# Kernel optimization log

Measured on AMD Instinct MI355X. Metric: run time of the kernel, lower is better.

The kernel has to match this reference:

```python
import jax, jax.numpy as jnp
import numpy as np

B = 4096
IN = 1024      # input_shape * 2
H = 2048       # rnn_hidden_dim * 2
A = 64         # n_actions
A2 = A * A     # fc2 output width


def setup_inputs() -> dict:
    key = jax.random.key(0)
    ks = jax.random.split(key, 12)
    s_in = 1.0 / np.sqrt(IN)
    s_h = 1.0 / np.sqrt(H)
    return {
        "inputs": jax.random.normal(ks[0], (B, IN), jnp.float32),
        "hidden_state": jax.random.normal(ks[1], (B, H), jnp.float32),
        # fc1: Linear(IN -> H)
        "W1": jax.random.uniform(ks[2], (H, IN), jnp.float32, -s_in, s_in),
        "b1": jax.random.uniform(ks[3], (H,), jnp.float32, -s_in, s_in),
        # GRUCell(H -> H), gate order r, z, n
        "Wih": jax.random.uniform(ks[4], (3 * H, H), jnp.float32, -s_h, s_h),
        "Whh": jax.random.uniform(ks[5], (3 * H, H), jnp.float32, -s_h, s_h),
        "bih": jax.random.uniform(ks[6], (3 * H,), jnp.float32, -s_h, s_h),
        "bhh": jax.random.uniform(ks[7], (3 * H,), jnp.float32, -s_h, s_h),
        # fc2: Linear(H -> A^2)
        "W2": jax.random.uniform(ks[8], (A2, H), jnp.float32, -s_h, s_h),
        "b2": jax.random.uniform(ks[9], (A2,), jnp.float32, -s_h, s_h),
    }


# Static gather indices for the vectorized __decode_combined_output.
# Row 2i, col j: max over q[i, j : j+A]  (contiguous window)
_IDX1 = np.arange(A)[:, None] + np.arange(A)[None, :]              # [A, A]
# Row 2i+1, col j: max over q[i, k-1] for k in range(j, A^2, A);
# at j=0 the index k-1 = -1 wraps to the last element (torch semantics).
_IDX2 = (np.arange(A)[:, None] + np.arange(A)[None, :] * A - 1) % A2  # [A, A]


def reference(inputs, hidden_state, W1, b1, Wih, Whh, bih, bhh, W2, b2):
    x = jax.nn.relu(inputs @ W1.T + b1)                 # [B, H]
    h_in = hidden_state.reshape(-1, H)
    gi = x @ Wih.T + bih                                # [B, 3H]
    gh = h_in @ Whh.T + bhh                             # [B, 3H]
    ir, iz, inn = jnp.split(gi, 3, axis=1)
    hr, hz, hn = jnp.split(gh, 3, axis=1)
    r = jax.nn.sigmoid(ir + hr)
    z = jax.nn.sigmoid(iz + hz)
    n = jnp.tanh(inn + r * hn)
    h = (1.0 - z) * n + z * h_in                        # [B, H]
    q = h @ W2.T + b2                                   # [B, A^2]
    q1 = jnp.max(q[:, _IDX1], axis=-1)                  # [B, A]
    q2 = jnp.max(q[:, _IDX2], axis=-1)                  # [B, A]
    out = jnp.stack([q1, q2], axis=1).reshape(-1, A)    # interleaved [2B, A]
    return out, h
```

## Files before the change

### kernel.cpp

```cpp
#include <hip/hip_runtime.h>
#include <stdint.h>

typedef unsigned short u16;
typedef __bf16 bf16x8 __attribute__((ext_vector_type(8)));
typedef float f32x4 __attribute__((ext_vector_type(4)));
typedef u16 u16x8 __attribute__((ext_vector_type(8)));

__device__ __forceinline__ float b2f(u16 v) {
    union { float f; unsigned int u; } x; x.u = ((unsigned int)v) << 16; return x.f;
}
__device__ __forceinline__ u16 f2b(float f) {
    union { float f; unsigned int u; } x; x.f = f;
    unsigned int r = x.u + 0x7fff + ((x.u >> 16) & 1);
    return (u16)(r >> 16);
}

__device__ __forceinline__ void gll16(const void* g, void* l) {
    __builtin_amdgcn_global_load_lds(
        (const __attribute__((address_space(1))) void*)g,
        (__attribute__((address_space(3))) void*)l,
        16, 0, 0);
}

__device__ __forceinline__ bf16x8 pack8(float4 f0, float4 f1) {
    union { float4 f; uint4 u; } a, b;
    a.f = f0; b.f = f1;
    const unsigned sel = 0x07060302u;
    union { unsigned u[4]; bf16x8 v; } r;
    r.u[0] = __builtin_amdgcn_perm(a.u.y + 0x8000u, a.u.x + 0x8000u, sel);
    r.u[1] = __builtin_amdgcn_perm(a.u.w + 0x8000u, a.u.z + 0x8000u, sel);
    r.u[2] = __builtin_amdgcn_perm(b.u.y + 0x8000u, b.u.x + 0x8000u, sel);
    r.u[3] = __builtin_amdgcn_perm(b.u.w + 0x8000u, b.u.z + 0x8000u, sel);
    return r.v;
}

__global__ __launch_bounds__(256) void cvt_kernel(
    const float* __restrict__ s, u16* __restrict__ d)
{
    const size_t i = ((size_t)blockIdx.x * 256 + threadIdx.x) * 8;
    float4 f0 = *(const float4*)(s + i);
    float4 f1 = *(const float4*)(s + i + 4);
    union { bf16x8 v; u16x8 u; } r;
    r.v = pack8(f0, f1);
    *(u16x8*)(d + i) = r.u;
}


#define FBAR() do { asm volatile("" ::: "memory"); \
                    __builtin_amdgcn_s_barrier();  \
                    asm volatile("" ::: "memory"); } while (0)
#define WAIT_LGKM0() asm volatile("s_waitcnt lgkmcnt(0)" ::: "memory")
#define WAIT_VM6()   asm volatile("s_waitcnt vmcnt(6)" ::: "memory")
#define WAIT_VM0()   asm volatile("s_waitcnt vmcnt(0)" ::: "memory")

__device__ __forceinline__ void stage_half(
    const u16* __restrict__ Mp, int rowBase, int K, int k0,
    u16* region, int t, int w)
{
#pragma unroll
    for (int it = 0; it < 2; ++it) {
        const int phys = it * 512 + t;
        const int r = phys >> 3;
        const int c = (phys & 7) ^ (r & 7);
        gll16(Mp + (size_t)(rowBase + r) * K + (k0 + c * 8),
              (char*)region + (it * 512 + w * 64) * 16);
    }
}

__device__ __forceinline__ void ld_a(const u16* region, int ra, int g0,
                                     bf16x8 (&out)[4][2])
{
#pragma unroll
    for (int mi = 0; mi < 4; ++mi)
#pragma unroll
        for (int s = 0; s < 2; ++s) {
            const int lr = mi * 32 + ra;
            out[mi][s] = *(const bf16x8*)((const char*)region +
                         (lr * 8 + ((s * 4 + g0) ^ (lr & 7))) * 16);
        }
}

__device__ __forceinline__ void ld_b(const u16* region, int rb, int g0,
                                     bf16x8 (&out)[2][2])
{
#pragma unroll
    for (int ni = 0; ni < 2; ++ni)
#pragma unroll
        for (int s = 0; s < 2; ++s) {
            const int lr = ni * 64 + rb;
            out[ni][s] = *(const bf16x8*)((const char*)region +
                         (lr * 8 + ((s * 4 + g0) ^ (lr & 7))) * 16);
        }
}

template <int MO, int NO>
__device__ __forceinline__ void mfma_quad(const bf16x8 (&af)[4][2],
                                          const bf16x8 (&bf)[2][2],
                                          f32x4 (&acc)[8][4])
{
    __builtin_amdgcn_s_setprio(1);
#pragma unroll
    for (int mi = 0; mi < 4; ++mi)
#pragma unroll
        for (int ni = 0; ni < 2; ++ni)
#pragma unroll
            for (int s = 0; s < 2; ++s)
                acc[MO + mi][NO + ni] = __builtin_amdgcn_mfma_f32_16x16x32_bf16(
                    af[mi][s], bf[ni][s], acc[MO + mi][NO + ni], 0, 0, 0);
    __builtin_amdgcn_s_setprio(0);
}

template <bool RELU>
__global__ __launch_bounds__(512, 2) void gemm256(
    const u16* __restrict__ A, const u16* __restrict__ Bw,
    const float* __restrict__ bias, u16* __restrict__ C,
    int M, int N, int K)
{
    (void)M;
    __shared__ alignas(16) u16 L[2][4][8192];

    const int t = threadIdx.x;
    const int l = t & 63;
    const int w = t >> 6;
    const int wr = w >> 2;
    const int wc = w & 3;

    const int gx = gridDim.x;
    const int nwg = gx * gridDim.y;
    const int orig = blockIdx.y * gx + blockIdx.x;
    const int q8 = nwg >> 3, r8 = nwg & 7;
    const int xcd = orig & 7, rem = orig >> 3;
    const int wg = (xcd < r8 ? xcd * (q8 + 1)
                             : r8 * (q8 + 1) + (xcd - r8) * q8) + rem;
    const int mBase = (wg / gx) * 256;
    const int nBase = (wg % gx) * 256;

    const int frow = l & 15;
    const int g0 = l >> 4;
    const int ra = wr * 16 + frow;
    const int rb = wc * 16 + frow;

    f32x4 acc[8][4] = {};
    bf16x8 a0[4][2], a1[4][2], b0[2][2], b1[2][2];

    const int NI = K >> 7;

    stage_half(A,  mBase,       K, 0,  &L[0][0][0], t, w);
    stage_half(Bw, nBase,       K, 0,  &L[0][2][0], t, w);
    stage_half(Bw, nBase + 128, K, 0,  &L[0][3][0], t, w);
    stage_half(A,  mBase + 128, K, 0,  &L[0][1][0], t, w);
    stage_half(A,  mBase,       K, 64, &L[1][0][0], t, w);
    stage_half(Bw, nBase,       K, 64, &L[1][2][0], t, w);
    stage_half(Bw, nBase + 128, K, 64, &L[1][3][0], t, w);
    WAIT_VM6();
    FBAR();

    for (int i = 0; i < NI; ++i) {
        const bool nl = (i + 1 < NI);
        const int kT1 = (2 * i + 1) << 6;
        const int kT2 = (2 * i + 2) << 6;
        const int kT3 = (2 * i + 3) << 6;

        ld_a(&L[0][0][0], ra, g0, a0);
        ld_b(&L[0][2][0], rb, g0, b0);
        stage_half(A, mBase + 128, K, kT1, &L[1][1][0], t, w);
        FBAR();
        WAIT_LGKM0();
        mfma_quad<0, 0>(a0, b0, acc);
        FBAR();

        ld_b(&L[0][3][0], rb, g0, b1);
        if (nl) stage_half(A, mBase, K, kT2, &L[0][0][0], t, w);
        FBAR();
        WAIT_LGKM0();
        mfma_quad<0, 2>(a0, b1, acc);
        FBAR();

        ld_a(&L[0][1][0], ra, g0, a1);
        if (nl) stage_half(Bw, nBase, K, kT2, &L[0][2][0], t, w);
        FBAR();
        WAIT_LGKM0();
        mfma_quad<4, 0>(a1, b0, acc);
        FBAR();

        if (nl) stage_half(Bw, nBase + 128, K, kT2, &L[0][3][0], t, w);
        FBAR();
        mfma_quad<4, 2>(a1, b1, acc);
        if (nl) { WAIT_VM6(); } else { WAIT_VM0(); }
        FBAR();

        ld_a(&L[1][0][0], ra, g0, a0);
        ld_b(&L[1][2][0], rb, g0, b0);
        if (nl) stage_half(A, mBase + 128, K, kT2, &L[0][1][0], t, w);
        FBAR();
        WAIT_LGKM0();
        mfma_quad<0, 0>(a0, b0, acc);
        FBAR();

        ld_b(&L[1][3][0], rb, g0, b1);
        if (nl) stage_half(A, mBase, K, kT3, &L[1][0][0], t, w);
        FBAR();
        WAIT_LGKM0();
        mfma_quad<0, 2>(a0, b1, acc);
        FBAR();

        ld_a(&L[1][1][0], ra, g0, a1);
        if (nl) stage_half(Bw, nBase, K, kT3, &L[1][2][0], t, w);
        FBAR();
        WAIT_LGKM0();
        mfma_quad<4, 0>(a1, b0, acc);
        FBAR();

        if (nl) stage_half(Bw, nBase + 128, K, kT3, &L[1][3][0], t, w);
        FBAR();
        mfma_quad<4, 2>(a1, b1, acc);
        if (nl) { WAIT_VM6(); }
        FBAR();
    }

    const int rq = (l >> 4) * 4;
#pragma unroll
    for (int ni = 0; ni < 4; ++ni) {
        const int col = nBase + ni * 64 + wc * 16 + (l & 15);
        const float bv = bias[col];
#pragma unroll
        for (int mi = 0; mi < 8; ++mi) {
            const int row = mBase + mi * 32 + wr * 16 + rq;
#pragma unroll
            for (int i2 = 0; i2 < 4; ++i2) {
                float v = acc[mi][ni][i2] + bv;
                if (RELU) v = fmaxf(v, 0.0f);
                C[(size_t)(row + i2) * N + col] = f2b(v);
            }
        }
    }
}

__global__ __launch_bounds__(256) void gru_kernel(
    const u16* __restrict__ gi, const u16* __restrict__ gh,
    const float* __restrict__ hprev, float* __restrict__ houtf,
    u16* __restrict__ houtb, int H)
{
    const size_t idx = ((size_t)blockIdx.x * 256 + threadIdx.x) * 8;
    const size_t b = idx / H;
    const size_t j = idx - b * H;
    const size_t g0 = b * (size_t)(3 * H) + j;

    u16x8 vir = *(const u16x8*)&gi[g0];
    u16x8 viz = *(const u16x8*)&gi[g0 + H];
    u16x8 vin = *(const u16x8*)&gi[g0 + 2 * H];
    u16x8 vhr = *(const u16x8*)&gh[g0];
    u16x8 vhz = *(const u16x8*)&gh[g0 + H];
    u16x8 vhn = *(const u16x8*)&gh[g0 + 2 * H];
    float4 hp0 = *(const float4*)&hprev[idx];
    float4 hp1 = *(const float4*)&hprev[idx + 4];
    float hp[8] = {hp0.x, hp0.y, hp0.z, hp0.w, hp1.x, hp1.y, hp1.z, hp1.w};
    float ho[8];
    u16x8 ob;
#pragma unroll
    for (int i = 0; i < 8; ++i) {
        float r = 1.f / (1.f + expf(-(b2f(vir[i]) + b2f(vhr[i]))));
        float z = 1.f / (1.f + expf(-(b2f(viz[i]) + b2f(vhz[i]))));
        float n = tanhf(b2f(vin[i]) + r * b2f(vhn[i]));
        float h = (1.f - z) * n + z * hp[i];
        ho[i] = h;
        ob[i] = f2b(h);
    }
    *(float4*)&houtf[idx]     = make_float4(ho[0], ho[1], ho[2], ho[3]);
    *(float4*)&houtf[idx + 4] = make_float4(ho[4], ho[5], ho[6], ho[7]);
    *(u16x8*)&houtb[idx] = ob;
}

__global__ __launch_bounds__(256) void decode_kernel(
    const u16* __restrict__ q, float* __restrict__ out)
{
    __shared__ float s[4096];
    const int row = blockIdx.x;
    const int t = threadIdx.x;
    const size_t base = (size_t)row * 4096;
#pragma unroll
    for (int i = 0; i < 16; ++i) {
        int j = t + i * 256;
        s[j] = b2f(q[base + j]);
    }
    __syncthreads();
    if (t < 64) {
        float m = -INFINITY;
#pragma unroll 8
        for (int k = 0; k < 64; ++k) m = fmaxf(m, s[t + k]);
        out[(size_t)(2 * row) * 64 + t] = m;
    } else if (t < 128) {
        const int rr = t - 64;
        float m = -INFINITY;
#pragma unroll 8
        for (int k = 0; k < 64; ++k) m = fmaxf(m, s[rr + 64 * k]);
        const int j = (rr + 1) & 63;
        out[(size_t)(2 * row + 1) * 64 + j] = m;
    }
}

extern "C" void kernel_launch(void* const* d_in, const int* in_sizes, int n_in,
                              void* d_out, int out_size, void* d_ws, size_t ws_size,
                              hipStream_t stream) {
    constexpr int Bn = 4096, IN = 1024, H = 2048, A = 64, A2 = A * A;
    constexpr size_t BH  = (size_t)Bn * H;
    constexpr size_t H3H = (size_t)3 * H * H;
    constexpr size_t HIN = (size_t)H * IN;
    constexpr size_t BIN = (size_t)Bn * IN;
    constexpr size_t A2H = (size_t)A2 * H;
    constexpr size_t B3H = (size_t)Bn * 3 * H;
    constexpr size_t BA2 = (size_t)Bn * A2;

    const float* inputs = (const float*)d_in[0];
    const float* h0     = (const float*)d_in[1];
    const float* W1     = (const float*)d_in[2];
    const float* b1     = (const float*)d_in[3];
    const float* Wih    = (const float*)d_in[4];
    const float* Whh    = (const float*)d_in[5];
    const float* bih    = (const float*)d_in[6];
    const float* bhh    = (const float*)d_in[7];
    const float* W2     = (const float*)d_in[8];
    const float* b2     = (const float*)d_in[9];

    float* out  = (float*)d_out;
    float* hout = out + (size_t)2 * Bn * A;

    u16* wsu  = (u16*)d_ws;
    u16* h0b  = wsu;
    u16* Whhb = wsu + BH;
    u16* Wihb = wsu;
    u16* W1b  = wsu + H3H;
    u16* inb  = wsu + H3H + HIN;
    u16* x    = wsu + BH + H3H;
    u16* gi   = x + BH;
    u16* gh   = gi + B3H;
    u16* hbf  = gh + B3H;
    u16* q    = gi;
    u16* W2b  = gi + BA2;

    dim3 blk(256);
    dim3 gblk(512);
    cvt_kernel<<<dim3(BH  / 2048), blk, 0, stream>>>(h0,  h0b);
    cvt_kernel<<<dim3(H3H / 2048), blk, 0, stream>>>(Whh, Whhb);
    gemm256<false><<<dim3(3 * H / 256, Bn / 256), gblk, 0, stream>>>(
        h0b, Whhb, bhh, gh, Bn, 3 * H, H);
    cvt_kernel<<<dim3(HIN / 2048), blk, 0, stream>>>(W1, W1b);
    cvt_kernel<<<dim3(BIN / 2048), blk, 0, stream>>>(inputs, inb);
    cvt_kernel<<<dim3(H3H / 2048), blk, 0, stream>>>(Wih, Wihb);
    gemm256<true><<<dim3(H / 256, Bn / 256), gblk, 0, stream>>>(
        inb, W1b, b1, x, Bn, H, IN);
    gemm256<false><<<dim3(3 * H / 256, Bn / 256), gblk, 0, stream>>>(
        x, Wihb, bih, gi, Bn, 3 * H, H);
    gru_kernel<<<dim3((Bn * H / 8) / 256), blk, 0, stream>>>(
        gi, gh, h0, hout, hbf, H);
    cvt_kernel<<<dim3(A2H / 2048), blk, 0, stream>>>(W2, W2b);
    gemm256<false><<<dim3(A2 / 256, Bn / 256), gblk, 0, stream>>>(
        hbf, W2b, b2, q, Bn, A2, H);
    decode_kernel<<<dim3(Bn), blk, 0, stream>>>(q, out);
}
```

Baseline: 576.1 us.

## Fuse weight conversions into GEMM launches and remap tiles per XCD

Adds a mega_kernel whose first blocks run a GEMM while the remaining blocks convert fp32 weights and inputs to bf16. The W1, inputs and Wih conversions now ride along with the Whh GEMM, and the W2 conversion rides along with the Wih GEMM, which removes separate launches and lets memory-bound conversion overlap compute-bound GEMM. The tile-to-block mapping also changes: each XCD now owns a contiguous 2D region of output tiles, for better L2 locality. The workspace layout is reshuffled to avoid aliasing between buffers that are now live at the same time. Risks are that conversion blocks compete with GEMM blocks for CUs and bandwidth, and that the new region mapping assumes the grid divides evenly by 2 and 4.

```diff
diff --git a/kernel.cpp b/kernel.cpp
--- a/kernel.cpp
+++ b/kernel.cpp
@@ -111,12 +111,11 @@
 }
 
 template <bool RELU>
-__global__ __launch_bounds__(512, 2) void gemm256(
+__device__ __forceinline__ void gemm_body(
     const u16* __restrict__ A, const u16* __restrict__ Bw,
     const float* __restrict__ bias, u16* __restrict__ C,
-    int M, int N, int K)
-{
-    (void)M;
+    int N, int K, int gy, int gx, int bid)
+{
     __shared__ alignas(16) u16 L[2][4][8192];
 
     const int t = threadIdx.x;
@@ -125,15 +124,11 @@
     const int wr = w >> 2;
     const int wc = w & 3;
 
-    const int gx = gridDim.x;
-    const int nwg = gx * gridDim.y;
-    const int orig = blockIdx.y * gx + blockIdx.x;
-    const int q8 = nwg >> 3, r8 = nwg & 7;
-    const int xcd = orig & 7, rem = orig >> 3;
-    const int wg = (xcd < r8 ? xcd * (q8 + 1)
-                             : r8 * (q8 + 1) + (xcd - r8) * q8) + rem;
-    const int mBase = (wg / gx) * 256;
-    const int nBase = (wg % gx) * 256;
+    const int xcd = bid & 7, rem = bid >> 3;
+    const int rrows = gy >> 1, rcols = gx >> 2;
+    const int lr_ = rem / rcols, lc_ = rem % rcols;
+    const int mBase = ((xcd >> 2) * rrows + lr_) * 256;
+    const int nBase = ((xcd & 3) * rcols + lc_) * 256;
 
     const int frow = l & 15;
     const int g0 = l >> 4;
@@ -234,6 +229,42 @@
             }
         }
     }
+}
+
+template <bool RELU>
+__global__ __launch_bounds__(512, 2) void gemm256(
+    const u16* __restrict__ A, const u16* __restrict__ Bw,
+    const float* __restrict__ bias, u16* __restrict__ C,
+    int N, int K, int gy, int gx)
+{
+    gemm_body<RELU>(A, Bw, bias, C, N, K, gy, gx, blockIdx.x);
+}
+
+__global__ __launch_bounds__(512, 2) void mega_kernel(
+    const u16* __restrict__ A, const u16* __restrict__ Bw,
+    const float* __restrict__ bias, u16* __restrict__ C,
+    int N, int K, int gy, int gx,
+    const float* __restrict__ s0, u16* __restrict__ d0, int n0,
+    const float* __restrict__ s1, u16* __restrict__ d1, int n1,
+    const float* __restrict__ s2, u16* __restrict__ d2, int n2)
+{
+    const int gemmBlocks = gy * gx;
+    const int bid = blockIdx.x;
+    if (bid < gemmBlocks) {
+        gemm_body<false>(A, Bw, bias, C, N, K, gy, gx, bid);
+        return;
+    }
+    int cb = bid - gemmBlocks;
+    const float* s; u16* d;
+    if (cb < n0)            { s = s0; d = d0; }
+    else if (cb < n0 + n1)  { cb -= n0; s = s1; d = d1; }
+    else                    { cb -= n0 + n1; s = s2; d = d2; }
+    const size_t i = ((size_t)cb * 512 + threadIdx.x) * 8;
+    float4 f0 = *(const float4*)(s + i);
+    float4 f1 = *(const float4*)(s + i + 4);
+    union { bf16x8 v; u16x8 u; } r;
+    r.v = pack8(f0, f1);
+    *(u16x8*)(d + i) = r.u;
 }
 
 __global__ __launch_bounds__(256) void gru_kernel(
@@ -309,7 +340,6 @@
     constexpr size_t BIN = (size_t)Bn * IN;
     constexpr size_t A2H = (size_t)A2 * H;
     constexpr size_t B3H = (size_t)Bn * 3 * H;
-    constexpr size_t BA2 = (size_t)Bn * A2;
 
     const float* inputs = (const float*)d_in[0];
     const float* h0     = (const float*)d_in[1];
@@ -328,33 +358,42 @@
     u16* wsu  = (u16*)d_ws;
     u16* h0b  = wsu;
     u16* Whhb = wsu + BH;
-    u16* Wihb = wsu;
-    u16* W1b  = wsu + H3H;
-    u16* inb  = wsu + H3H + HIN;
-    u16* x    = wsu + BH + H3H;
-    u16* gi   = x + BH;
-    u16* gh   = gi + B3H;
-    u16* hbf  = gh + B3H;
-    u16* q    = gi;
-    u16* W2b  = gi + BA2;
+    u16* gi   = wsu;
+    u16* q    = wsu;
+    u16* gh   = wsu + B3H;
+    u16* Wihb = wsu + 2 * B3H;
+    u16* hbf  = wsu + 2 * B3H;
+    u16* W1b  = wsu + 2 * B3H + H3H;
+    u16* inb  = W1b + HIN;
+    u16* xb   = inb + BIN;
+    u16* W2b  = xb + BH;
 
     dim3 blk(256);
     dim3 gblk(512);
+
     cvt_kernel<<<dim3(BH  / 2048), blk, 0, stream>>>(h0,  h0b);
     cvt_kernel<<<dim3(H3H / 2048), blk, 0, stream>>>(Whh, Whhb);
-    gemm256<false><<<dim3(3 * H / 256, Bn / 256), gblk, 0, stream>>>(
-        h0b, Whhb, bhh, gh, Bn, 3 * H, H);
-    cvt_kernel<<<dim3(HIN / 2048), blk, 0, stream>>>(W1, W1b);
-    cvt_kernel<<<dim3(BIN / 2048), blk, 0, stream>>>(inputs, inb);
-    cvt_kernel<<<dim3(H3H / 2048), blk, 0, stream>>>(Wih, Wihb);
-    gemm256<true><<<dim3(H / 256, Bn / 256), gblk, 0, stream>>>(
-        inb, W1b, b1, x, Bn, H, IN);
-    gemm256<false><<<dim3(3 * H / 256, Bn / 256), gblk, 0, stream>>>(
-        x, Wihb, bih, gi, Bn, 3 * H, H);
+
+    mega_kernel<<<dim3(16 * 24 + 512 + 1024 + 3072), gblk, 0, stream>>>(
+        h0b, Whhb, bhh, gh, 3 * H, H, 16, 24,
+        W1,     W1b,  (int)(HIN / 4096),
+        inputs, inb,  (int)(BIN / 4096),
+        Wih,    Wihb, (int)(H3H / 4096));
+
+    gemm256<true><<<dim3(16 * 8), gblk, 0, stream>>>(
+        inb, W1b, b1, xb, H, IN, 16, 8);
+
+    mega_kernel<<<dim3(16 * 24 + 2048), gblk, 0, stream>>>(
+        xb, Wihb, bih, gi, 3 * H, H, 16, 24,
+        W2, W2b, (int)(A2H / 4096),
+        W2, W2b, 0,
+        W2, W2b, 0);
+
     gru_kernel<<<dim3((Bn * H / 8) / 256), blk, 0, stream>>>(
         gi, gh, h0, hout, hbf, H);
-    cvt_kernel<<<dim3(A2H / 2048), blk, 0, stream>>>(W2, W2b);
-    gemm256<false><<<dim3(A2 / 256, Bn / 256), gblk, 0, stream>>>(
-        hbf, W2b, b2, q, Bn, A2, H);
+
+    gemm256<false><<<dim3(16 * 16), gblk, 0, stream>>>(
+        hbf, W2b, b2, q, A2, H, 16, 16);
+
     decode_kernel<<<dim3(Bn), blk, 0, stream>>>(q, out);
 }
```

Result: faster. 530.5 us (-7.9%).
